# Kernel optimization log

Hardware: AMD Instinct MI355X
Metric: run time of the kernel (lower is better)

## Reference

```python
import jax, jax.numpy as jnp
import numpy as np

N, L, D, H = 2, 2048, 1024, 16
DK = D // H  # 64


def setup_inputs() -> dict:
    key = jax.random.key(0)
    ks = jax.random.split(key, 8)
    Xq = jax.random.normal(ks[0], (N, L, D), dtype=jnp.float32)
    Xk = jax.random.normal(ks[1], (N, L, D), dtype=jnp.float32)
    Xv = jax.random.normal(ks[2], (N, L, D), dtype=jnp.float32)
    mask_2d = jax.random.randint(ks[3], (N, L, L), 0, 2, dtype=jnp.int32)
    scale = 0.02
    Wq = jax.random.normal(ks[4], (D, D), dtype=jnp.float32) * scale
    Wk = jax.random.normal(ks[5], (D, D), dtype=jnp.float32) * scale
    Wv = jax.random.normal(ks[6], (D, D), dtype=jnp.float32) * scale
    Wo = jax.random.normal(ks[7], (D, D), dtype=jnp.float32) * scale
    return {"Xq": Xq, "Xk": Xk, "Xv": Xv, "Wq": Wq, "Wk": Wk, "Wv": Wv, "Wo": Wo, "mask_2d": mask_2d}


def reference(Xq, Xk, Xv, Wq, Wk, Wv, Wo, mask_2d):
    # Projections (bias=False). Per-head slicing in the original == reshape to [N,L,H,DK].
    Q = (Xq @ Wq).reshape(N, L, H, DK)
    K = (Xk @ Wk).reshape(N, L, H, DK)
    V = (Xv @ Wv).reshape(N, L, H, DK)
    # Scaled dot-product scores: [N, H, L, L]
    scores = jnp.einsum("blhd,bmhd->bhlm", Q, K) / jnp.sqrt(jnp.asarray(DK, scores_dtype(Q)))
    # NOTE: original uses masked_fill(mask==0, 0) BEFORE softmax (zero-fill, not -inf).
    scores = jnp.where(mask_2d[:, None, :, :] == 0, jnp.zeros((), scores.dtype), scores)
    A = jax.nn.softmax(scores, axis=-1)
    O = jnp.einsum("bhlm,bmhd->blhd", A, V).reshape(N, L, D)
    return O @ Wo


def scores_dtype(Q):
    return Q.dtype
```

## Files before the change

### kernel.cpp

```cpp
#include <hip/hip_runtime.h>
#include <hip/hip_bf16.h>

#define NB 2
#define L_SEQ 2048
#define NH 16
#define DKH 64
#define DMODEL 1024
#define MROWS (NB * L_SEQ)
#define QSCALE 0.18033688f
#define DD (DMODEL * DMODEL)

typedef __attribute__((ext_vector_type(8))) short short8;
typedef __attribute__((ext_vector_type(4))) float f32x4;

static __device__ __forceinline__ unsigned short f2bf(float f) {
    unsigned u = __float_as_uint(f);
    u += 0x7fffu + ((u >> 16) & 1u);
    return (unsigned short)(u >> 16);
}

static __device__ __forceinline__ float fexp2(float x) {
#if __has_builtin(__builtin_amdgcn_exp2f)
    return __builtin_amdgcn_exp2f(x);
#else
    return __expf(x * 0.6931471806f);
#endif
}

static __device__ __forceinline__ unsigned pk_bf16(float a, float b) {
    __hip_bfloat162 h = __float22bfloat162_rn(make_float2(a, b));
    return *reinterpret_cast<unsigned*>(&h);
}

static __device__ __forceinline__ void gll16(const void* g, void* l) {
    __builtin_amdgcn_global_load_lds(
        (const __attribute__((address_space(1))) void*)g,
        (__attribute__((address_space(3))) void*)l, 16, 0, 0);
}

__global__ __launch_bounds__(256)
void prep(const float* __restrict__ Xq, const float* __restrict__ Xk,
          const float* __restrict__ Xv, const float* __restrict__ w0,
          const float* __restrict__ w1, const float* __restrict__ w2,
          const float* __restrict__ w3, const int* __restrict__ mask,
          unsigned short* __restrict__ XB, unsigned short* __restrict__ WtB,
          unsigned long long* __restrict__ MWT)
{
    __shared__ float ts[32][33];
    const int bx = blockIdx.x;
    const int t  = threadIdx.x;

    if (bx < 12288) {
        const int z = bx >> 12;
        const float* src = (z == 0) ? Xq : (z == 1) ? Xk : Xv;
        const size_t i4 = (size_t)(bx & 4095) * 256 + t;
        float4 v = ((const float4*)src)[i4];
        ushort4 o;
        o.x = f2bf(v.x); o.y = f2bf(v.y); o.z = f2bf(v.z); o.w = f2bf(v.w);
        ((ushort4*)(XB + (size_t)z * 4194304))[i4] = o;
    } else if (bx < 16384) {
        const int idx = bx - 12288;
        const int z   = idx >> 10;
        const int rem = idx & 1023;
        const float* W = (z == 0) ? w0 : (z == 1) ? w1 : (z == 2) ? w2 : w3;
        unsigned short* Wt = WtB + (size_t)z * DD;
        const int n0 = (rem & 31) * 32;
        const int k0 = (rem >> 5) * 32;
        const int r  = t >> 3;
        const int c  = (t & 7) * 4;
        float4 v = *(const float4*)&W[(size_t)(k0 + r) * DMODEL + n0 + c];
        ts[r][c + 0] = v.x; ts[r][c + 1] = v.y;
        ts[r][c + 2] = v.z; ts[r][c + 3] = v.w;
        __syncthreads();
        ushort4 o;
        o.x = f2bf(ts[c + 0][r]); o.y = f2bf(ts[c + 1][r]);
        o.z = f2bf(ts[c + 2][r]); o.w = f2bf(ts[c + 3][r]);
        *(ushort4*)&Wt[(size_t)(n0 + r) * DMODEL + k0 + c] = o;
    } else {
        const int lane = t & 63;
        const size_t wbase = (size_t)(bx - 16384) * 4 + (t >> 6);
#pragma unroll
        for (int it = 0; it < 8; ++it) {
            const size_t wid = wbase + (size_t)it * 16384;
            const int mv = mask[wid * 64 + lane];
            const unsigned long long bits = __ballot(mv != 0);
            if (lane == 0) {
                const int b   = (int)(wid >> 16);
                const int rem = (int)(wid & 65535);
                const int row = rem >> 5;
                const int wd  = rem & 31;
                MWT[((size_t)b * 32 + wd) * L_SEQ + row] = bits;
            }
        }
    }
}

__global__ __launch_bounds__(256)
void gemm_qkv(const unsigned short* __restrict__ XB,
              const unsigned short* __restrict__ WtB,
              unsigned short* __restrict__ QKV)
{
    __shared__ __align__(16) unsigned short SMEM[16384];

    const int t    = threadIdx.x;
    const int w    = t >> 6;
    const int lane = t & 63;

    const int bid   = blockIdx.x;
    const int xcd   = bid & 7;
    const int idx   = bid >> 3;
    const int pair  = xcd * 12 + (idx >> 3);
    const int n0    = (idx & 7) * 128;
    const int m0    = (pair & 31) * 128;
    const int z     = pair >> 5;

    const unsigned short* A = XB  + (size_t)z * ((size_t)MROWS * DMODEL);
    const unsigned short* B = WtB + (size_t)z * DD;

    const int srow = lane >> 2;
    const int sc4  = (lane & 3) ^ (srow & 3);

    const unsigned short* ag[2];
    const unsigned short* bg[2];
    int lao[2], lbo[2];
#pragma unroll
    for (int g = 0; g < 2; ++g) {
        const int R = w * 32 + g * 16;
        ag[g] = A + (size_t)(m0 + R + srow) * DMODEL + sc4 * 8;
        bg[g] = B + (size_t)(n0 + R + srow) * DMODEL + sc4 * 8;
        lao[g] = R * 32;
        lbo[g] = R * 32;
    }

    const int ml = lane & 15;
    const int q  = lane >> 4;
    const int wm = (w >> 1) * 64;
    const int wn = (w & 1) * 64;

    const f32x4 z4 = {0.f, 0.f, 0.f, 0.f};
    f32x4 acc[4][4];
#pragma unroll
    for (int i = 0; i < 4; ++i)
#pragma unroll
        for (int j = 0; j < 4; ++j) acc[i][j] = z4;

#pragma unroll
    for (int g = 0; g < 2; ++g) {
        gll16(ag[g], &SMEM[lao[g]]);
        gll16(bg[g], &SMEM[8192 + lbo[g]]);
    }

    for (int j = 0; j < 32; ++j) {
        const int cur = j & 1;
        __syncthreads();
        if (j < 31) {
            const int kt = (j + 1) * 32;
            const int nb = (cur ^ 1) * 4096;
#pragma unroll
            for (int g = 0; g < 2; ++g) {
                gll16(ag[g] + kt, &SMEM[nb + lao[g]]);
                gll16(bg[g] + kt, &SMEM[8192 + nb + lbo[g]]);
            }
        }
        const unsigned short* As = &SMEM[cur * 4096];
        const unsigned short* Bs = &SMEM[8192 + cur * 4096];
        short8 av[4], bv[4];
#pragma unroll
        for (int mt = 0; mt < 4; ++mt)
            av[mt] = *(const short8*)
                &As[(wm + mt * 16 + ml) * 32 + ((q ^ (ml & 3)) * 8)];
#pragma unroll
        for (int nt = 0; nt < 4; ++nt)
            bv[nt] = *(const short8*)
                &Bs[(wn + nt * 16 + ml) * 32 + ((q ^ (ml & 3)) * 8)];
#pragma unroll
        for (int mt = 0; mt < 4; ++mt)
#pragma unroll
            for (int nt = 0; nt < 4; ++nt)
                acc[mt][nt] = __builtin_amdgcn_mfma_f32_16x16x32_bf16(
                    av[mt], bv[nt], acc[mt][nt], 0, 0, 0);
    }

    unsigned short* O = QKV + (size_t)z * ((size_t)MROWS * DMODEL);
    __syncthreads();
    unsigned short* Ts = SMEM;

    if (z == 2) {
#pragma unroll
        for (int mt = 0; mt < 4; ++mt) {
            const int trow0 = wm + mt * 16 + q * 4;
            const int ch    = trow0 >> 3;
#pragma unroll
            for (int nt = 0; nt < 4; ++nt) {
                const int tcol = wn + nt * 16 + ml;
                const int pc   = (ch & 8) | ((ch & 7) ^ (tcol & 7));
                ushort4 pv;
                pv.x = f2bf(acc[mt][nt][0]); pv.y = f2bf(acc[mt][nt][1]);
                pv.z = f2bf(acc[mt][nt][2]); pv.w = f2bf(acc[mt][nt][3]);
                *(ushort4*)&Ts[tcol * 128 + pc * 8 + (trow0 & 7)] = pv;
            }
        }
        __syncthreads();
        const int bb = m0 >> 11;
        const int l0 = (m0 & (L_SEQ - 1)) + (t & 15) * 8;
        const int cr = t & 15;
#pragma unroll
        for (int it = 0; it < 8; ++it) {
            const int tcol = (t >> 4) + 16 * it;
            const int pc   = (cr & 8) | ((cr & 7) ^ (tcol & 7));
            short8 vv = *(const short8*)&Ts[tcol * 128 + pc * 8];
            const int n  = n0 + tcol;
            const int hh = n >> 6;
            const int dk = n & (DKH - 1);
            *(short8*)&O[((size_t)(bb * NH + hh) * DKH + dk) * L_SEQ + l0] = vv;
        }
    } else {
        const float qs = (z == 0) ? QSCALE : 1.0f;
#pragma unroll
        for (int mt = 0; mt < 4; ++mt) {
            const int row0 = wm + mt * 16 + q * 4;
#pragma unroll
            for (int nt = 0; nt < 4; ++nt) {
                const int col = wn + nt * 16 + ml;
#pragma unroll
                for (int r = 0; r < 4; ++r)
                    Ts[(row0 + r) * 128 + col] = f2bf(acc[mt][nt][r] * qs);
            }
        }
        __syncthreads();
        const int mloc = t >> 3;
        const int c0   = t & 7;
#pragma unroll
        for (int pass = 0; pass < 4; ++pass) {
#pragma unroll
            for (int half = 0; half < 2; ++half) {
                const int m = mloc + 32 * pass;
                const int c = c0 + 8 * half;
                short8 v = *(const short8*)&Ts[m * 128 + c * 8];
                const int row = m0 + m;
                const int bb  = row >> 11;
                const int l   = row & (L_SEQ - 1);
                const int n   = n0 + c * 8;
                const int hh  = n >> 6;
                const int dk  = n & (DKH - 1);
                *(short8*)&O[(((size_t)(bb * NH + hh) * L_SEQ + l) << 6) + dk] = v;
            }
        }
    }
}

__global__ __launch_bounds__(256)
void gemm_out(const unsigned short* __restrict__ OB,
              const unsigned short* __restrict__ Wt,
              float* __restrict__ out)
{
    __shared__ __align__(16) unsigned short As[2][2048];
    __shared__ __align__(16) unsigned short Bs[2][4096];

    const int t    = threadIdx.x;
    const int w    = t >> 6;
    const int lane = t & 63;

    const int bid = blockIdx.x;
    const int xcd = bid & 7;
    const int idx = bid >> 3;
    const int n0  = (idx & 7) * 128;
    const int m0  = (xcd * 8 + (idx >> 3)) * 64;

    const int srow = lane >> 2;
    const int sc4  = (lane & 3) ^ (srow & 3);

    const unsigned short* ag =
        OB + (size_t)(m0 + w * 16 + srow) * DMODEL + sc4 * 8;
    const unsigned short* bg[2];
    int lbo[2];
#pragma unroll
    for (int g = 0; g < 2; ++g) {
        const int R = w * 32 + g * 16;
        bg[g] = Wt + (size_t)(n0 + R + srow) * DMODEL + sc4 * 8;
        lbo[g] = R * 32;
    }
    const int lao = (w * 16) * 32;

    const int ml = lane & 15;
    const int q  = lane >> 4;
    const int wm = (w >> 1) * 32;
    const int wn = (w & 1) * 64;

    const f32x4 z4 = {0.f, 0.f, 0.f, 0.f};
    f32x4 acc[2][4];
#pragma unroll
    for (int i = 0; i < 2; ++i)
#pragma unroll
        for (int j = 0; j < 4; ++j) acc[i][j] = z4;

    gll16(ag, &As[0][lao]);
#pragma unroll
    for (int g = 0; g < 2; ++g) gll16(bg[g], &Bs[0][lbo[g]]);

    for (int j = 0; j < 32; ++j) {
        const int cur = j & 1;
        __syncthreads();
        if (j < 31) {
            const int kt = (j + 1) * 32;
            gll16(ag + kt, &As[cur ^ 1][lao]);
#pragma unroll
            for (int g = 0; g < 2; ++g)
                gll16(bg[g] + kt, &Bs[cur ^ 1][lbo[g]]);
        }
        short8 av[2], bv[4];
#pragma unroll
        for (int mt = 0; mt < 2; ++mt)
            av[mt] = *(const short8*)
                &As[cur][(wm + mt * 16 + ml) * 32 + ((q ^ (ml & 3)) * 8)];
#pragma unroll
        for (int nt = 0; nt < 4; ++nt)
            bv[nt] = *(const short8*)
                &Bs[cur][(wn + nt * 16 + ml) * 32 + ((q ^ (ml & 3)) * 8)];
#pragma unroll
        for (int mt = 0; mt < 2; ++mt)
#pragma unroll
            for (int nt = 0; nt < 4; ++nt)
                acc[mt][nt] = __builtin_amdgcn_mfma_f32_16x16x32_bf16(
                    av[mt], bv[nt], acc[mt][nt], 0, 0, 0);
    }

#pragma unroll
    for (int mt = 0; mt < 2; ++mt) {
        const int gr0 = m0 + wm + mt * 16 + q * 4;
#pragma unroll
        for (int nt = 0; nt < 4; ++nt) {
            const int col = n0 + wn + nt * 16 + ml;
#pragma unroll
            for (int r = 0; r < 4; ++r)
                out[(size_t)(gr0 + r) * DMODEL + col] = acc[mt][nt][r];
        }
    }
}

__global__ __launch_bounds__(256, 2)
void attn_mfma(const unsigned short* __restrict__ Qb,
               const unsigned short* __restrict__ Kb,
               const unsigned short* __restrict__ Vtb,
               const unsigned long long* __restrict__ MWT,
               unsigned short* __restrict__ OB)
{
    __shared__ __align__(16) unsigned short Ks[2][64 * 64];
    __shared__ __align__(16) unsigned short Vts[2][64 * 64];
    __shared__ __align__(16) unsigned short Ps[4][32 * 64];
    __shared__ __align__(16) unsigned long long MskL[2][128];

    const int t    = threadIdx.x;
    const int w    = t >> 6;
    const int lane = t & 63;
    const int ml   = lane & 15;
    const int quad = lane >> 4;

    const int bid = blockIdx.x;
    const int xcd = bid & 7;
    const int idx = bid >> 3;
    const int p   = xcd * 4 + (idx >> 4);
    const int jq  = idx & 15;
    const int h   = p & 15;
    const int b   = p >> 4;
    const int q0  = jq * 128;

    const size_t hoff = (size_t)(b * NH + h) * L_SEQ * DKH;
    const unsigned short* Qh  = Qb  + hoff;
    const unsigned short* Kh  = Kb  + hoff;
    const unsigned short* Vth = Vtb + hoff;

    const int srow = lane >> 3;
    const int sc   = (lane & 7) ^ srow;

    unsigned short* QL = &Ks[0][0];
#pragma unroll
    for (int g = 0; g < 4; ++g)
        gll16(Qh + (size_t)(q0 + w * 32 + g * 8 + srow) * DKH + sc * 8,
              &QL[(w * 32 + g * 8) * 64]);

    const unsigned short* kg0 = Kh + (size_t)(w * 16 + srow) * DKH + sc * 8;
    const unsigned short* kg1 = Kh + (size_t)(w * 16 + 8 + srow) * DKH + sc * 8;
    const unsigned short* vg0 = Vth + (size_t)(w * 16 + srow) * L_SEQ + sc * 8;
    const unsigned short* vg1 = Vth + (size_t)(w * 16 + 8 + srow) * L_SEQ + sc * 8;

    short8 kr0 = *(const short8*)kg0;  kg0 += 64 * DKH;
    short8 kr1 = *(const short8*)kg1;  kg1 += 64 * DKH;
    short8 vr0 = *(const short8*)vg0;  vg0 += 64;
    short8 vr1 = *(const short8*)vg1;  vg1 += 64;

    const unsigned long long* mg = MWT + (size_t)b * 32 * L_SEQ + q0 + t;
    unsigned long long m_pf = 0;
    if (t < 128) m_pf = mg[0];

    __syncthreads();

    short8 qf[2][2];
#pragma unroll
    for (int qn = 0; qn < 2; ++qn)
#pragma unroll
        for (int s = 0; s < 2; ++s)
            qf[qn][s] = *(const short8*)
                &QL[(w * 32 + qn * 16 + ml) * 64 +
                    (((s * 4 + quad) ^ (ml & 7)) * 8)];

    __syncthreads();

    *(short8*)&Ks[0][(w * 16) * 64 + lane * 8]      = kr0;
    *(short8*)&Ks[0][(w * 16 + 8) * 64 + lane * 8]  = kr1;
    *(short8*)&Vts[0][(w * 16) * 64 + lane * 8]     = vr0;
    *(short8*)&Vts[0][(w * 16 + 8) * 64 + lane * 8] = vr1;
    if (t < 128) MskL[0][t] = m_pf;

    kr0 = *(const short8*)kg0;  kg0 += 64 * DKH;
    kr1 = *(const short8*)kg1;  kg1 += 64 * DKH;
    vr0 = *(const short8*)vg0;  vg0 += 64;
    vr1 = *(const short8*)vg1;  vg1 += 64;
    if (t < 128) m_pf = mg[L_SEQ];

    f32x4 oacc[2][4];
    const f32x4 z4 = {0.f, 0.f, 0.f, 0.f};
#pragma unroll
    for (int qn = 0; qn < 2; ++qn)
#pragma unroll
        for (int dt = 0; dt < 4; ++dt) oacc[qn][dt] = z4;
    float l_i[2] = {0.f, 0.f};

    __syncthreads();

    for (int j = 0; j < 32; ++j) {
        const int cur = j & 1;
        if (j < 31) {
            const int nxt = cur ^ 1;
            *(short8*)&Ks[nxt][(w * 16) * 64 + lane * 8]      = kr0;
            *(short8*)&Ks[nxt][(w * 16 + 8) * 64 + lane * 8]  = kr1;
            *(short8*)&Vts[nxt][(w * 16) * 64 + lane * 8]     = vr0;
            *(short8*)&Vts[nxt][(w * 16 + 8) * 64 + lane * 8] = vr1;
            if (t < 128) MskL[nxt][t] = m_pf;
            if (j < 30) {
                kr0 = *(const short8*)kg0;  kg0 += 64 * DKH;
                kr1 = *(const short8*)kg1;  kg1 += 64 * DKH;
                vr0 = *(const short8*)vg0;  vg0 += 64;
                vr1 = *(const short8*)vg1;  vg1 += 64;
                if (t < 128) m_pf = mg[(size_t)(j + 2) * L_SEQ];
            }
        }

        f32x4 sacc[2][4];
#pragma unroll
        for (int qn = 0; qn < 2; ++qn)
#pragma unroll
            for (int kt = 0; kt < 4; ++kt) sacc[qn][kt] = z4;
#pragma unroll
        for (int s = 0; s < 2; ++s) {
            short8 kf[4];
#pragma unroll
            for (int kt = 0; kt < 4; ++kt)
                kf[kt] = *(const short8*)
                    &Ks[cur][(kt * 16 + ml) * 64 +
                             (((s * 4 + quad) ^ (ml & 7)) * 8)];
#pragma unroll
            for (int qn = 0; qn < 2; ++qn)
#pragma unroll
                for (int kt = 0; kt < 4; ++kt)
                    sacc[qn][kt] = __builtin_amdgcn_mfma_f32_16x16x32_bf16(
                        kf[kt], qf[qn][s], sacc[qn][kt], 0, 0, 0);
        }

#pragma unroll
        for (int qn = 0; qn < 2; ++qn) {
            const unsigned long long wq =
                MskL[cur][w * 32 + qn * 16 + ml] >> (quad * 4);
            const unsigned mlo = (unsigned)wq;
            const unsigned mhi = (unsigned)(wq >> 32);
            float rs = 0.f;
            float pr[4][4];
#pragma unroll
            for (int kt = 0; kt < 4; ++kt) {
                const unsigned word = (kt < 2) ? mlo : mhi;
                const int base = (kt & 1) * 16;
#pragma unroll
                for (int r = 0; r < 4; ++r) {
                    const float mf = (float)((word >> (base + r)) & 1u);
                    const float e  = fexp2(sacc[qn][kt][r] * mf);
                    pr[kt][r] = e;
                    rs += e;
                }
            }
            rs += __shfl_xor(rs, 16);
            rs += __shfl_xor(rs, 32);
            l_i[qn] += rs;
#pragma unroll
            for (int kt = 0; kt < 4; ++kt) {
                uint2 pk;
                pk.x = pk_bf16(pr[kt][0], pr[kt][1]);
                pk.y = pk_bf16(pr[kt][2], pr[kt][3]);
                const int cp = (kt * 2 + (quad >> 1)) ^ (ml & 7);
                *(uint2*)&Ps[w][(qn * 16 + ml) * 64 + cp * 8 + (quad & 1) * 4] = pk;
            }
        }

#pragma unroll
        for (int s = 0; s < 2; ++s) {
            short8 vf[4];
#pragma unroll
            for (int dt = 0; dt < 4; ++dt)
                vf[dt] = *(const short8*)
                    &Vts[cur][(dt * 16 + ml) * 64 +
                              (((s * 4 + quad) ^ (ml & 7)) * 8)];
#pragma unroll
            for (int qn = 0; qn < 2; ++qn) {
                const short8 pf = *(const short8*)
                    &Ps[w][(qn * 16 + ml) * 64 +
                           (((s * 4 + quad) ^ (ml & 7)) * 8)];
#pragma unroll
                for (int dt = 0; dt < 4; ++dt)
                    oacc[qn][dt] = __builtin_amdgcn_mfma_f32_16x16x32_bf16(
                        vf[dt], pf, oacc[qn][dt], 0, 0, 0);
            }
        }

        __syncthreads();
    }

#pragma unroll
    for (int qn = 0; qn < 2; ++qn) {
        const float inv = 1.0f / l_i[qn];
        const int qrow = q0 + w * 32 + qn * 16 + ml;
#pragma unroll
        for (int dt = 0; dt < 4; ++dt) {
            ushort4 o4;
            o4.x = f2bf(oacc[qn][dt][0] * inv);
            o4.y = f2bf(oacc[qn][dt][1] * inv);
            o4.z = f2bf(oacc[qn][dt][2] * inv);
            o4.w = f2bf(oacc[qn][dt][3] * inv);
            *(ushort4*)&OB[(size_t)(b * L_SEQ + qrow) * DMODEL + h * DKH +
                           dt * 16 + quad * 4] = o4;
        }
    }
}

extern "C" void kernel_launch(void* const* d_in, const int* in_sizes, int n_in,
                              void* d_out, int out_size, void* d_ws, size_t ws_size,
                              hipStream_t stream)
{
    (void)in_sizes; (void)n_in; (void)out_size; (void)ws_size;

    const float* Xq   = (const float*)d_in[0];
    const float* Xk   = (const float*)d_in[1];
    const float* Xv   = (const float*)d_in[2];
    const float* Wq   = (const float*)d_in[3];
    const float* Wk   = (const float*)d_in[4];
    const float* Wv   = (const float*)d_in[5];
    const float* Wo   = (const float*)d_in[6];
    const int*   mask = (const int*)d_in[7];
    float* out = (float*)d_out;

    char* base = (char*)d_ws;
    unsigned short*     XB  = (unsigned short*)base;
    unsigned short*     WtB = (unsigned short*)(base + (24u << 20));
    unsigned short*     QKV = (unsigned short*)(base + (32u << 20));
    unsigned short*     OB  = (unsigned short*)(base + (56u << 20));
    unsigned long long* MWT = (unsigned long long*)(base + (64u << 20));

    const size_t tsz = (size_t)MROWS * DMODEL;

    prep<<<dim3(20480), 256, 0, stream>>>(
        Xq, Xk, Xv, Wq, Wk, Wv, Wo, mask, XB, WtB, MWT);

    gemm_qkv<<<dim3(768), 256, 0, stream>>>(XB, WtB, QKV);

    attn_mfma<<<dim3(512), 256, 0, stream>>>(
        QKV, QKV + tsz, QKV + 2 * tsz, MWT, OB);

    gemm_out<<<dim3(512), 256, 0, stream>>>(OB, WtB + 3 * (size_t)DD, out);
}
```

Before: 261.2 us.

## Keep P in registers via permlane swaps instead of LDS round-trip

The softmax probabilities are now rearranged into the MFMA B-operand layout with permlane32/permlane16 swaps instead of being written to shared memory and read back, which removes the P LDS buffer and its traffic. The per-tile cross-lane row-sum reduction is deferred to a single reduction before the final normalization. The mask multiply is replaced by a sign-extended bitfield AND on the score bits. The permlane fallback uses shuffles and selects, and correctness depends on the swap pattern matching the MFMA operand layout.

```diff
diff --git a/kernel.cpp b/kernel.cpp
--- a/kernel.cpp
+++ b/kernel.cpp
@@ -12,6 +12,8 @@
 
 typedef __attribute__((ext_vector_type(8))) short short8;
 typedef __attribute__((ext_vector_type(4))) float f32x4;
+typedef __attribute__((ext_vector_type(2))) int int2v;
+typedef __attribute__((ext_vector_type(4))) int int4v;
 
 static __device__ __forceinline__ unsigned short f2bf(float f) {
     unsigned u = __float_as_uint(f);
@@ -36,6 +38,42 @@
     __builtin_amdgcn_global_load_lds(
         (const __attribute__((address_space(1))) void*)g,
         (__attribute__((address_space(3))) void*)l, 16, 0, 0);
+}
+
+static __device__ __forceinline__ int2v pl32swap(int a, int b) {
+#if __has_builtin(__builtin_amdgcn_permlane32_swap)
+    return __builtin_amdgcn_permlane32_swap(a, b, false, false);
+#else
+    const int pa = __shfl_xor(a, 32);
+    const int pb = __shfl_xor(b, 32);
+    const bool lo = ((threadIdx.x & 63) < 32);
+    int2v r;
+    r.x = lo ? a : pb;
+    r.y = lo ? pa : b;
+    return r;
+#endif
+}
+
+static __device__ __forceinline__ int2v pl16swap(int a, int b) {
+#if __has_builtin(__builtin_amdgcn_permlane16_swap)
+    return __builtin_amdgcn_permlane16_swap(a, b, false, false);
+#else
+    const int pa = __shfl_xor(a, 16);
+    const int pb = __shfl_xor(b, 16);
+    const bool ev = (((threadIdx.x >> 4) & 1) == 0);
+    int2v r;
+    r.x = ev ? a : pb;
+    r.y = ev ? pa : b;
+    return r;
+#endif
+}
+
+static __device__ __forceinline__ int sbfe1(int word, int off) {
+#if __has_builtin(__builtin_amdgcn_sbfe)
+    return __builtin_amdgcn_sbfe(word, off, 1);
+#else
+    return (word << (31 - off)) >> 31;
+#endif
 }
 
 __global__ __launch_bounds__(256)
@@ -347,7 +385,6 @@
 {
     __shared__ __align__(16) unsigned short Ks[2][64 * 64];
     __shared__ __align__(16) unsigned short Vts[2][64 * 64];
-    __shared__ __align__(16) unsigned short Ps[4][32 * 64];
     __shared__ __align__(16) unsigned long long MskL[2][128];
 
     const int t    = threadIdx.x;
@@ -467,6 +504,7 @@
                         kf[kt], qf[qn][s], sacc[qn][kt], 0, 0, 0);
         }
 
+        short8 pfq[2][2];
 #pragma unroll
         for (int qn = 0; qn < 2; ++qn) {
             const unsigned long long wq =
@@ -477,26 +515,35 @@
             float pr[4][4];
 #pragma unroll
             for (int kt = 0; kt < 4; ++kt) {
-                const unsigned word = (kt < 2) ? mlo : mhi;
+                const int word = (int)((kt < 2) ? mlo : mhi);
                 const int base = (kt & 1) * 16;
 #pragma unroll
                 for (int r = 0; r < 4; ++r) {
-                    const float mf = (float)((word >> (base + r)) & 1u);
-                    const float e  = fexp2(sacc[qn][kt][r] * mf);
+                    const int mm = sbfe1(word, base + r);
+                    const float sm =
+                        __int_as_float(__float_as_int(sacc[qn][kt][r]) & mm);
+                    const float e = fexp2(sm);
                     pr[kt][r] = e;
                     rs += e;
                 }
             }
-            rs += __shfl_xor(rs, 16);
-            rs += __shfl_xor(rs, 32);
             l_i[qn] += rs;
+
+            int p01[4], p23[4];
 #pragma unroll
             for (int kt = 0; kt < 4; ++kt) {
-                uint2 pk;
-                pk.x = pk_bf16(pr[kt][0], pr[kt][1]);
-                pk.y = pk_bf16(pr[kt][2], pr[kt][3]);
-                const int cp = (kt * 2 + (quad >> 1)) ^ (ml & 7);
-                *(uint2*)&Ps[w][(qn * 16 + ml) * 64 + cp * 8 + (quad & 1) * 4] = pk;
+                p01[kt] = (int)pk_bf16(pr[kt][0], pr[kt][1]);
+                p23[kt] = (int)pk_bf16(pr[kt][2], pr[kt][3]);
+            }
+#pragma unroll
+            for (int s = 0; s < 2; ++s) {
+                const int2v w01 = pl32swap(p01[2 * s], p01[2 * s + 1]);
+                const int2v r01 = pl16swap(w01.x, w01.y);
+                const int2v w23 = pl32swap(p23[2 * s], p23[2 * s + 1]);
+                const int2v r23 = pl16swap(w23.x, w23.y);
+                int4v pw;
+                pw.x = r01.x; pw.y = r23.x; pw.z = r01.y; pw.w = r23.y;
+                pfq[qn][s] = __builtin_bit_cast(short8, pw);
             }
         }
 
@@ -509,15 +556,11 @@
                     &Vts[cur][(dt * 16 + ml) * 64 +
                               (((s * 4 + quad) ^ (ml & 7)) * 8)];
 #pragma unroll
-            for (int qn = 0; qn < 2; ++qn) {
-                const short8 pf = *(const short8*)
-                    &Ps[w][(qn * 16 + ml) * 64 +
-                           (((s * 4 + quad) ^ (ml & 7)) * 8)];
+            for (int qn = 0; qn < 2; ++qn)
 #pragma unroll
                 for (int dt = 0; dt < 4; ++dt)
                     oacc[qn][dt] = __builtin_amdgcn_mfma_f32_16x16x32_bf16(
-                        vf[dt], pf, oacc[qn][dt], 0, 0, 0);
-            }
+                        vf[dt], pfq[qn][s], oacc[qn][dt], 0, 0, 0);
         }
 
         __syncthreads();
@@ -525,7 +568,10 @@
 
 #pragma unroll
     for (int qn = 0; qn < 2; ++qn) {
-        const float inv = 1.0f / l_i[qn];
+        float l = l_i[qn];
+        l += __shfl_xor(l, 16);
+        l += __shfl_xor(l, 32);
+        const float inv = 1.0f / l;
         const int qrow = q0 + w * 32 + qn * 16 + ml;
 #pragma unroll
         for (int dt = 0; dt < 4; ++dt) {
```

Result: faster. 250.6 us (-4.1%).
